# Kernel optimization log

Measured on AMD Instinct MI355X. Metric: run time of the kernel, lower is better.

Reference implementation:

```python
import jax, jax.numpy as jnp
import numpy as np

# Dims: C cells, L gene tokens, E embed, H mlp hidden, M factors, K topk
C, L, E, H, M, K = 16, 8192, 512, 256, 128, 30
TAU = 1.0        # gumbel-softmax temperature
SOFTNESS = 0.01  # soft-mask sharpness
TEMP = 1.0       # logits temperature
EPS = 1e-20


def setup_inputs() -> dict:
    key = jax.random.key(0)
    ks = jax.random.split(key, 7)
    x = jax.random.normal(ks[0], (C, L, E), dtype=jnp.float32)
    key_padding_mask = jax.random.randint(ks[1], (C, L), 0, 2) > 0  # True = valid
    uniform_noise = jax.random.uniform(ks[2], (C, L - 1, M), dtype=jnp.float32)
    W1 = jax.random.normal(ks[3], (E, H), dtype=jnp.float32) * (1.0 / np.sqrt(E))
    b1 = jnp.zeros((H,), dtype=jnp.float32)
    W2 = jax.random.normal(ks[4], (H, M), dtype=jnp.float32) * (1.0 / np.sqrt(H))
    b2 = jnp.zeros((M,), dtype=jnp.float32)
    return {"x": x, "key_padding_mask": key_padding_mask,
            "uniform_noise": uniform_noise,
            "W1": W1, "b1": b1, "W2": W2, "b2": b2}


def reference(x, key_padding_mask, uniform_noise, W1, b1, W2, b2):
    # default gene_subset: drop token 0, keep the rest  -> S = L-1
    xs = x[:, 1:, :]                          # (C, S, E)
    kpm = key_padding_mask[:, 1:]             # (C, S)

    # 2-layer MLP router (dropout p=0 -> identity)
    h = jax.nn.relu(jnp.einsum('cse,eh->csh', xs, W1) + b1)   # (C, S, H)
    logits = (jnp.einsum('csh,hm->csm', h, W2) + b2) / TEMP    # (C, S, M)

    # GumbelTopK, training path: gumbel-softmax then smooth top-k mask
    gumbel = -jnp.log(-jnp.log(uniform_noise + EPS) + EPS)
    perturbed = (logits + gumbel) / TAU
    probs = jax.nn.softmax(perturbed, axis=-1)                 # (C, S, M)
    topk_vals, _ = jax.lax.top_k(probs, K)                     # (C, S, K)
    threshold = topk_vals[..., -1:]                            # (C, S, 1)
    smooth_mask = jax.nn.sigmoid((probs - threshold) / SOFTNESS)
    out = probs * smooth_mask

    # faithful to the source: mask = ~key_padding_mask; probs *= mask
    out = out * (~kpm)[..., None].astype(out.dtype)
    return out, kpm
```

## Files before the change

### kernel.cpp

```cpp
#include <hip/hip_runtime.h>
#include <hip/hip_bf16.h>

#define CC 16
#define LL 8192
#define SS 8191
#define EE 512
#define HH 256
#define MM 128
#define TOPK 30

typedef __attribute__((ext_vector_type(8))) short short8;
typedef __attribute__((ext_vector_type(4))) float f32x4;
typedef __attribute__((ext_vector_type(4))) unsigned int u32x4;

static __device__ __forceinline__ unsigned short f2bf(float f) {
    unsigned u = __builtin_bit_cast(unsigned, f);
    u += 0x7FFFu + ((u >> 16) & 1u);
    return (unsigned short)(u >> 16);
}

static __device__ __forceinline__ unsigned pk2(float lo, float hi) {
    __hip_bfloat162 t = __float22bfloat162_rn(float2{lo, hi});
    unsigned u;
    __builtin_memcpy(&u, &t, 4);
    return u;
}

static __device__ __forceinline__ short8 cvt8(const float4 a, const float4 b) {
    u32x4 uv;
    uv[0] = pk2(a.x, a.y);
    uv[1] = pk2(a.z, a.w);
    uv[2] = pk2(b.x, b.y);
    uv[3] = pk2(b.z, b.w);
    return __builtin_bit_cast(short8, uv);
}

static __device__ __forceinline__ void gl2lds16(const float* g, unsigned char* l) {
    __builtin_amdgcn_global_load_lds(
        (const __attribute__((address_space(1))) void*)g,
        (__attribute__((address_space(3))) void*)l,
        16, 0, 0);
}

template<int CTRL>
static __device__ __forceinline__ float dppf(float v) {
    return __builtin_bit_cast(float,
        __builtin_amdgcn_update_dpp(0, __builtin_bit_cast(int, v), CTRL, 0xF, 0xF, false));
}
template<int CTRL>
static __device__ __forceinline__ int dppi(int v) {
    return __builtin_amdgcn_update_dpp(0, v, CTRL, 0xF, 0xF, false);
}
static __device__ __forceinline__ float sum16f(float v) {
    v += dppf<0x121>(v); v += dppf<0x122>(v); v += dppf<0x124>(v); v += dppf<0x128>(v);
    return v;
}
static __device__ __forceinline__ float max16f(float v) {
    v = fmaxf(v, dppf<0x121>(v)); v = fmaxf(v, dppf<0x122>(v));
    v = fmaxf(v, dppf<0x124>(v)); v = fmaxf(v, dppf<0x128>(v));
    return v;
}
static __device__ __forceinline__ unsigned sum16u(unsigned v) {
    v += (unsigned)dppi<0x121>((int)v); v += (unsigned)dppi<0x122>((int)v);
    v += (unsigned)dppi<0x124>((int)v); v += (unsigned)dppi<0x128>((int)v);
    return v;
}

__global__ void prep_weights(const float* __restrict__ W1, const float* __restrict__ W2,
                             unsigned short* __restrict__ W1T, unsigned short* __restrict__ W2T)
{
    const int b = blockIdx.x, tid = threadIdx.x;
    if (b < 64) {
        const int e0 = b * 8, h = tid;
        short8 sv;
#pragma unroll
        for (int j = 0; j < 8; ++j)
            sv[j] = (short)f2bf(W1[(size_t)(e0 + j) * HH + h]);
        *(short8*)(void*)(W1T + (size_t)h * EE + e0) = sv;
    } else {
        const int h0 = (b - 64) * 16;
        if (tid < MM) {
            const int m = tid;
            short8 s0v, s1v;
#pragma unroll
            for (int j = 0; j < 8; ++j) {
                s0v[j] = (short)f2bf(W2[(size_t)(h0 + j) * MM + m]);
                s1v[j] = (short)f2bf(W2[(size_t)(h0 + 8 + j) * MM + m]);
            }
            *(short8*)(void*)(W2T + (size_t)m * HH + h0) = s0v;
            *(short8*)(void*)(W2T + (size_t)m * HH + h0 + 8) = s1v;
        }
    }
}

__global__ __launch_bounds__(512, 4)
void gene_router_kernel(const float* __restrict__ x,
                        const int*   __restrict__ mask,
                        const float* __restrict__ noise,
                        const unsigned short* __restrict__ W1T,
                        const float* __restrict__ b1,
                        const unsigned short* __restrict__ W2T,
                        const float* __restrict__ b2,
                        float* __restrict__ out,
                        float* __restrict__ outk)
{
    __shared__ __align__(16) unsigned char lds[65536];

    const int tid = threadIdx.x;
    const int c   = blockIdx.y;
    const int s0  = blockIdx.x * 128;

    const int w    = tid >> 6;
    const int lane = tid & 63;
    const int lr   = lane & 15;
    const int kq   = lane >> 4;
    const int wr   = w >> 2;
    const int wc   = w & 3;
    const int tx   = tid & 15;
    const int ty   = tid >> 4;

    if (tid < 128) {
        const int s = s0 + tid;
        if (s < SS)
            outk[(size_t)c * SS + s] = (mask[(size_t)c * LL + s + 1] != 0) ? 1.0f : 0.0f;
    }

    const float* xb = x + ((size_t)c * LL + s0 + 1) * EE;

#define STAGE(ck, bufoff) do {                                              \
    _Pragma("unroll")                                                       \
    for (int it_ = 0; it_ < 4; ++it_) {                                     \
        const int row_ = it_ * 32 + ty;                                     \
        const int rs_  = min(s0 + row_, SS - 1) - s0;                       \
        const float* g_ = xb + (size_t)rs_ * EE + (ck) * 64                 \
                          + ((tx ^ (row_ & 7)) << 2);                       \
        gl2lds16(g_, lds + (bufoff) + (it_ * 512 + tid) * 16);              \
    } } while (0)

    const int cw = wc * 64;
    float b1v[4];
#pragma unroll
    for (int n = 0; n < 4; ++n) b1v[n] = b1[cw + n * 16 + lr];

    f32x4 acc[4][4];
#pragma unroll
    for (int r = 0; r < 4; ++r)
#pragma unroll
        for (int n = 0; n < 4; ++n) acc[r][n] = (f32x4)0.0f;

    STAGE(0, 0);
    __syncthreads();

    for (int ck = 0; ck < 8; ++ck) {
        const int cur = (ck & 1) << 15;
        if (ck < 7) STAGE(ck + 1, ((ck + 1) & 1) << 15);
#pragma unroll
        for (int ks = 0; ks < 2; ++ks) {
            short8 af[4];
#pragma unroll
            for (int r = 0; r < 4; ++r) {
                const int row = wr * 64 + r * 16 + lr;
                const int ug  = ks * 8 + kq * 2;
                const float4 a0 = *(const float4*)(const void*)
                    (lds + cur + row * 256 + (((ug + 0) ^ (row & 7)) << 4));
                const float4 a1 = *(const float4*)(const void*)
                    (lds + cur + row * 256 + (((ug + 1) ^ (row & 7)) << 4));
                af[r] = cvt8(a0, a1);
            }
            short8 bf_[4];
#pragma unroll
            for (int n = 0; n < 4; ++n)
                bf_[n] = *(const short8*)(const void*)
                    (W1T + (size_t)(cw + n * 16 + lr) * EE + ck * 64 + ks * 32 + kq * 8);
#pragma unroll
            for (int r = 0; r < 4; ++r)
#pragma unroll
                for (int n = 0; n < 4; ++n)
                    acc[r][n] = __builtin_amdgcn_mfma_f32_16x16x32_bf16(af[r], bf_[n], acc[r][n], 0, 0, 0);
        }
        __syncthreads();
    }

#pragma unroll
    for (int n = 0; n < 4; ++n) {
        const int colh = cw + n * 16 + lr;
#pragma unroll
        for (int r = 0; r < 4; ++r)
#pragma unroll
            for (int q = 0; q < 4; ++q) {
                const int row = wr * 64 + r * 16 + kq * 4 + q;
                *(unsigned short*)(lds + row * 512 + ((colh * 2) ^ ((row & 7) << 4))) =
                    f2bf(fmaxf(acc[r][n][q] + b1v[n], 0.0f));
            }
    }
    __syncthreads();

    float4 nz[4][2];
    int mk[4];
#pragma unroll
    for (int i = 0; i < 4; ++i) {
        const int s  = s0 + ty * 4 + i;
        const int sc = min(s, SS - 1);
        const float* np_ = noise + ((size_t)c * SS + sc) * MM + tx * 8;
        nz[i][0] = *(const float4*)np_;
        nz[i][1] = *(const float4*)(np_ + 4);
        mk[i] = mask[(size_t)c * LL + sc + 1];
    }
    const float4 b2a = *(const float4*)(b2 + tx * 8);
    const float4 b2b = *(const float4*)(b2 + tx * 8 + 4);

    f32x4 acc2[4][2];
#pragma unroll
    for (int r = 0; r < 4; ++r)
#pragma unroll
        for (int n = 0; n < 2; ++n) acc2[r][n] = (f32x4)0.0f;

    const int cw2 = wc * 32;
#pragma unroll 4
    for (int ks = 0; ks < 8; ++ks) {
        short8 ah[4];
#pragma unroll
        for (int r = 0; r < 4; ++r) {
            const int row = wr * 64 + r * 16 + lr;
            ah[r] = *(const short8*)(const void*)
                (lds + row * 512 + ((ks * 64 + kq * 16) ^ ((row & 7) << 4)));
        }
        short8 bw[2];
#pragma unroll
        for (int n = 0; n < 2; ++n)
            bw[n] = *(const short8*)(const void*)
                (W2T + (size_t)(cw2 + n * 16 + lr) * HH + ks * 32 + kq * 8);
#pragma unroll
        for (int r = 0; r < 4; ++r)
#pragma unroll
            for (int n = 0; n < 2; ++n)
                acc2[r][n] = __builtin_amdgcn_mfma_f32_16x16x32_bf16(ah[r], bw[n], acc2[r][n], 0, 0, 0);
    }
    __syncthreads();

#pragma unroll
    for (int r = 0; r < 4; ++r)
#pragma unroll
        for (int n = 0; n < 2; ++n)
#pragma unroll
            for (int q = 0; q < 4; ++q) {
                const int row = wr * 64 + r * 16 + kq * 4 + q;
                const int col = cw2 + n * 16 + lr;
                *(float*)(lds + row * 512
                          + ((((col >> 2) << 4) ^ ((row & 7) << 4)) | ((col & 3) << 2)))
                    = acc2[r][n][q];
            }
    __syncthreads();

    float b2v[8] = {b2a.x, b2a.y, b2a.z, b2a.w, b2b.x, b2b.y, b2b.z, b2b.w};

    float pr[4][8];
    float pmaxv[4];
#pragma unroll
    for (int i = 0; i < 4; ++i) {
        const int row = ty * 4 + i;
        const float4 l0 = *(const float4*)(const void*)
            (lds + row * 512 + ((tx * 32) ^ ((row & 7) << 4)));
        const float4 l1 = *(const float4*)(const void*)
            (lds + row * 512 + ((tx * 32 + 16) ^ ((row & 7) << 4)));
        const float lg[8] = {l0.x, l0.y, l0.z, l0.w, l1.x, l1.y, l1.z, l1.w};
        const float uu[8] = {nz[i][0].x, nz[i][0].y, nz[i][0].z, nz[i][0].w,
                             nz[i][1].x, nz[i][1].y, nz[i][1].z, nz[i][1].w};
        float pm[8];
#pragma unroll
        for (int q = 0; q < 8; ++q) {
            const float g = -__logf(-__logf(uu[q] + 1e-20f) + 1e-20f);
            pm[q] = lg[q] + b2v[q] + g;
        }
        float mx = pm[0];
#pragma unroll
        for (int q = 1; q < 8; ++q) mx = fmaxf(mx, pm[q]);
        mx = max16f(mx);
        float se = 0.0f;
#pragma unroll
        for (int q = 0; q < 8; ++q) { pr[i][q] = __expf(pm[q] - mx); se += pr[i][q]; }
        se = sum16f(se);
        const float inv = 1.0f / se;
#pragma unroll
        for (int q = 0; q < 8; ++q) pr[i][q] *= inv;
        pmaxv[i] = inv;
    }

    float lo[4], hi[4];
#pragma unroll
    for (int i = 0; i < 4; ++i) { lo[i] = 0.0f; hi[i] = fminf(pmaxv[i], 1.0f / 30.0f); }
    for (int it = 0; it < 16; ++it) {
        float mid[4];
#pragma unroll
        for (int i = 0; i < 4; ++i) mid[i] = 0.5f * (lo[i] + hi[i]);
        unsigned cnt = 0;
#pragma unroll
        for (int q = 0; q < 8; ++q) {
            cnt += (pr[0][q] > mid[0]) ? 1u : 0u;
            cnt += (pr[1][q] > mid[1]) ? (1u << 8) : 0u;
            cnt += (pr[2][q] > mid[2]) ? (1u << 16) : 0u;
            cnt += (pr[3][q] > mid[3]) ? (1u << 24) : 0u;
        }
        cnt = sum16u(cnt);
#pragma unroll
        for (int i = 0; i < 4; ++i) {
            const bool ge = ((cnt >> (8 * i)) & 255u) >= TOPK;
            lo[i] = ge ? mid[i] : lo[i];
            hi[i] = ge ? hi[i] : mid[i];
        }
    }

#pragma unroll
    for (int i = 0; i < 4; ++i) {
        const int s = s0 + ty * 4 + i;
        if (s < SS) {
            const float mz = (mk[i] != 0) ? 0.0f : 1.0f;
            float ov[8];
#pragma unroll
            for (int q = 0; q < 8; ++q) {
                const float sm = 1.0f / (1.0f + __expf((hi[i] - pr[i][q]) * 100.0f));
                ov[q] = pr[i][q] * sm * mz;
            }
            float* op = out + ((size_t)c * SS + s) * MM + tx * 8;
            float4 o0, o1;
            o0.x=ov[0]; o0.y=ov[1]; o0.z=ov[2]; o0.w=ov[3];
            o1.x=ov[4]; o1.y=ov[5]; o1.z=ov[6]; o1.w=ov[7];
            *(float4*)(op + 0) = o0;
            *(float4*)(op + 4) = o1;
        }
    }
#undef STAGE
}

extern "C" void kernel_launch(void* const* d_in, const int* in_sizes, int n_in,
                              void* d_out, int out_size, void* d_ws, size_t ws_size,
                              hipStream_t stream) {
    const float* x     = (const float*)d_in[0];
    const int*   mask  = (const int*)d_in[1];
    const float* noise = (const float*)d_in[2];
    const float* W1    = (const float*)d_in[3];
    const float* b1    = (const float*)d_in[4];
    const float* W2    = (const float*)d_in[5];
    const float* b2    = (const float*)d_in[6];
    float* out  = (float*)d_out;
    float* outk = out + (size_t)CC * SS * MM;

    unsigned short* W1T = (unsigned short*)d_ws;
    unsigned short* W2T = W1T + (size_t)HH * EE;

    prep_weights<<<dim3(80), dim3(256), 0, stream>>>(W1, W2, W1T, W2T);

    dim3 grid(64, CC);
    gene_router_kernel<<<grid, dim3(512), 0, stream>>>(x, mask, noise, W1T, b1, W2T, b2, out, outk);
}
```

Measured before the change: 181.0 us.

## Deepen x staging to 4-buffer ring with vmcnt waits and lighter barriers

Replaces the double-buffered 64-column x staging with a 4-slot ring of 32-column chunks, keeping three chunks in flight and waiting with explicit s_waitcnt vmcnt counts instead of full syncthreads. Later __syncthreads calls become raw s_barrier plus an lgkmcnt wait with sched_barrier fences. The aim is to hide global-to-LDS latency behind the MFMA work and cut barrier overhead. In exchange there are twice as many barriers in the K loop, a hand-tuned wait schedule that must match the issued loads exactly, and reduced scheduler freedom.

```diff
diff --git a/kernel.cpp b/kernel.cpp
--- a/kernel.cpp
+++ b/kernel.cpp
@@ -64,6 +64,18 @@
     v += (unsigned)dppi<0x121>((int)v); v += (unsigned)dppi<0x122>((int)v);
     v += (unsigned)dppi<0x124>((int)v); v += (unsigned)dppi<0x128>((int)v);
     return v;
+}
+
+static __device__ __forceinline__ void bar_only() {
+    __builtin_amdgcn_sched_barrier(0);
+    __builtin_amdgcn_s_barrier();
+    __builtin_amdgcn_sched_barrier(0);
+}
+static __device__ __forceinline__ void bar_lgkm() {
+    asm volatile("s_waitcnt lgkmcnt(0)" ::: "memory");
+    __builtin_amdgcn_sched_barrier(0);
+    __builtin_amdgcn_s_barrier();
+    __builtin_amdgcn_sched_barrier(0);
 }
 
 __global__ void prep_weights(const float* __restrict__ W1, const float* __restrict__ W2,
@@ -127,14 +139,16 @@
 
     const float* xb = x + ((size_t)c * LL + s0 + 1) * EE;
 
-#define STAGE(ck, bufoff) do {                                              \
+#define STAGE(ck) do {                                                      \
+    const int bo_ = ((ck) & 3) * 16384;                                     \
     _Pragma("unroll")                                                       \
-    for (int it_ = 0; it_ < 4; ++it_) {                                     \
-        const int row_ = it_ * 32 + ty;                                     \
+    for (int j_ = 0; j_ < 2; ++j_) {                                        \
+        const int unit_ = j_ * 512 + tid;                                   \
+        const int row_ = unit_ >> 3, uu_ = unit_ & 7;                       \
         const int rs_  = min(s0 + row_, SS - 1) - s0;                       \
-        const float* g_ = xb + (size_t)rs_ * EE + (ck) * 64                 \
-                          + ((tx ^ (row_ & 7)) << 2);                       \
-        gl2lds16(g_, lds + (bufoff) + (it_ * 512 + tid) * 16);              \
+        const float* g_ = xb + (size_t)rs_ * EE + (ck) * 32                 \
+                          + ((uu_ ^ (row_ & 7)) << 2);                      \
+        gl2lds16(g_, lds + bo_ + unit_ * 16);                               \
     } } while (0)
 
     const int cw = wc * 64;
@@ -148,38 +162,44 @@
 #pragma unroll
         for (int n = 0; n < 4; ++n) acc[r][n] = (f32x4)0.0f;
 
-    STAGE(0, 0);
-    __syncthreads();
-
-    for (int ck = 0; ck < 8; ++ck) {
-        const int cur = (ck & 1) << 15;
-        if (ck < 7) STAGE(ck + 1, ((ck + 1) & 1) << 15);
-#pragma unroll
-        for (int ks = 0; ks < 2; ++ks) {
-            short8 af[4];
-#pragma unroll
-            for (int r = 0; r < 4; ++r) {
-                const int row = wr * 64 + r * 16 + lr;
-                const int ug  = ks * 8 + kq * 2;
-                const float4 a0 = *(const float4*)(const void*)
-                    (lds + cur + row * 256 + (((ug + 0) ^ (row & 7)) << 4));
-                const float4 a1 = *(const float4*)(const void*)
-                    (lds + cur + row * 256 + (((ug + 1) ^ (row & 7)) << 4));
-                af[r] = cvt8(a0, a1);
-            }
-            short8 bf_[4];
-#pragma unroll
-            for (int n = 0; n < 4; ++n)
-                bf_[n] = *(const short8*)(const void*)
-                    (W1T + (size_t)(cw + n * 16 + lr) * EE + ck * 64 + ks * 32 + kq * 8);
-#pragma unroll
-            for (int r = 0; r < 4; ++r)
-#pragma unroll
-                for (int n = 0; n < 4; ++n)
-                    acc[r][n] = __builtin_amdgcn_mfma_f32_16x16x32_bf16(af[r], bf_[n], acc[r][n], 0, 0, 0);
-        }
-        __syncthreads();
-    }
+    STAGE(0); STAGE(1); STAGE(2);
+
+#define DO_CHUNK(C, W) do {                                                 \
+    asm volatile("s_waitcnt vmcnt(" #W ")" ::: "memory");                   \
+    __builtin_amdgcn_sched_barrier(0);                                      \
+    __builtin_amdgcn_s_barrier();                                           \
+    __builtin_amdgcn_sched_barrier(0);                                      \
+    if ((C) < 13) STAGE((C) + 3);                                           \
+    const unsigned char* cb_ = lds + ((C) & 3) * 16384;                     \
+    short8 af_[4];                                                          \
+    _Pragma("unroll")                                                       \
+    for (int r_ = 0; r_ < 4; ++r_) {                                        \
+        const int row_ = wr * 64 + r_ * 16 + lr;                            \
+        const float4 a0_ = *(const float4*)(const void*)                    \
+            (cb_ + row_ * 128 + (((kq * 2 + 0) ^ (row_ & 7)) << 4));        \
+        const float4 a1_ = *(const float4*)(const void*)                    \
+            (cb_ + row_ * 128 + (((kq * 2 + 1) ^ (row_ & 7)) << 4));        \
+        af_[r_] = cvt8(a0_, a1_);                                           \
+    }                                                                       \
+    short8 bw_[4];                                                          \
+    _Pragma("unroll")                                                       \
+    for (int n_ = 0; n_ < 4; ++n_)                                          \
+        bw_[n_] = *(const short8*)(const void*)                             \
+            (W1T + (size_t)(cw + n_ * 16 + lr) * EE + (C) * 32 + kq * 8);   \
+    _Pragma("unroll")                                                       \
+    for (int r_ = 0; r_ < 4; ++r_)                                          \
+        _Pragma("unroll")                                                   \
+        for (int n_ = 0; n_ < 4; ++n_)                                      \
+            acc[r_][n_] = __builtin_amdgcn_mfma_f32_16x16x32_bf16(          \
+                af_[r_], bw_[n_], acc[r_][n_], 0, 0, 0);                    \
+    } while (0)
+
+    DO_CHUNK( 0, 4); DO_CHUNK( 1, 4); DO_CHUNK( 2, 4); DO_CHUNK( 3, 4);
+    DO_CHUNK( 4, 4); DO_CHUNK( 5, 4); DO_CHUNK( 6, 4); DO_CHUNK( 7, 4);
+    DO_CHUNK( 8, 4); DO_CHUNK( 9, 4); DO_CHUNK(10, 4); DO_CHUNK(11, 4);
+    DO_CHUNK(12, 4); DO_CHUNK(13, 4); DO_CHUNK(14, 2); DO_CHUNK(15, 0);
+
+    bar_only();
 
 #pragma unroll
     for (int n = 0; n < 4; ++n) {
@@ -193,7 +213,7 @@
                     f2bf(fmaxf(acc[r][n][q] + b1v[n], 0.0f));
             }
     }
-    __syncthreads();
+    bar_lgkm();
 
     float4 nz[4][2];
     int mk[4];
@@ -236,7 +256,7 @@
             for (int n = 0; n < 2; ++n)
                 acc2[r][n] = __builtin_amdgcn_mfma_f32_16x16x32_bf16(ah[r], bw[n], acc2[r][n], 0, 0, 0);
     }
-    __syncthreads();
+    bar_lgkm();
 
 #pragma unroll
     for (int r = 0; r < 4; ++r)
@@ -250,7 +270,7 @@
                           + ((((col >> 2) << 4) ^ ((row & 7) << 4)) | ((col & 3) << 2)))
                     = acc2[r][n][q];
             }
-    __syncthreads();
+    bar_lgkm();
 
     float b2v[8] = {b2a.x, b2a.y, b2a.z, b2a.w, b2b.x, b2b.y, b2b.z, b2b.w};
 
@@ -329,6 +349,7 @@
             *(float4*)(op + 4) = o1;
         }
     }
+#undef DO_CHUNK
 #undef STAGE
 }
 
```

Result: slower. 186.2 us (+2.9%).

## Split fused router into GEMM kernel and separate softmax/top-k epilogue kernel

Applied to the files above, without the earlier changes.

Splits the single fused kernel into two. The first does the MLP GEMMs and writes raw logits to the output buffer. The second reads logits and noise back and does the gumbel-softmax, the top-k threshold search and the masking. The aim is to shed register and LDS pressure from the epilogue in the GEMM kernel and run the epilogue at higher occupancy. The cost is an extra global round trip of the logits, about 67 MB. The bisection is also cut from 16 to 10 iterations, which coarsens the threshold and may change numerics.

```diff
diff --git a/kernel.cpp b/kernel.cpp
--- a/kernel.cpp
+++ b/kernel.cpp
@@ -8,6 +8,7 @@
 #define HH 256
 #define MM 128
 #define TOPK 30
+#define TOT (CC * SS)
 
 typedef __attribute__((ext_vector_type(8))) short short8;
 typedef __attribute__((ext_vector_type(4))) float f32x4;
@@ -94,15 +95,11 @@
 }
 
 __global__ __launch_bounds__(512, 4)
-void gene_router_kernel(const float* __restrict__ x,
-                        const int*   __restrict__ mask,
-                        const float* __restrict__ noise,
-                        const unsigned short* __restrict__ W1T,
-                        const float* __restrict__ b1,
-                        const unsigned short* __restrict__ W2T,
-                        const float* __restrict__ b2,
-                        float* __restrict__ out,
-                        float* __restrict__ outk)
+void gene_gemm_kernel(const float* __restrict__ x,
+                      const unsigned short* __restrict__ W1T,
+                      const float* __restrict__ b1,
+                      const unsigned short* __restrict__ W2T,
+                      float* __restrict__ logits)
 {
     __shared__ __align__(16) unsigned char lds[65536];
 
@@ -118,12 +115,6 @@
     const int wc   = w & 3;
     const int tx   = tid & 15;
     const int ty   = tid >> 4;
-
-    if (tid < 128) {
-        const int s = s0 + tid;
-        if (s < SS)
-            outk[(size_t)c * SS + s] = (mask[(size_t)c * LL + s + 1] != 0) ? 1.0f : 0.0f;
-    }
 
     const float* xb = x + ((size_t)c * LL + s0 + 1) * EE;
 
@@ -195,20 +186,6 @@
     }
     __syncthreads();
 
-    float4 nz[4][2];
-    int mk[4];
-#pragma unroll
-    for (int i = 0; i < 4; ++i) {
-        const int s  = s0 + ty * 4 + i;
-        const int sc = min(s, SS - 1);
-        const float* np_ = noise + ((size_t)c * SS + sc) * MM + tx * 8;
-        nz[i][0] = *(const float4*)np_;
-        nz[i][1] = *(const float4*)(np_ + 4);
-        mk[i] = mask[(size_t)c * LL + sc + 1];
-    }
-    const float4 b2a = *(const float4*)(b2 + tx * 8);
-    const float4 b2b = *(const float4*)(b2 + tx * 8 + 4);
-
     f32x4 acc2[4][2];
 #pragma unroll
     for (int r = 0; r < 4; ++r)
@@ -236,7 +213,6 @@
             for (int n = 0; n < 2; ++n)
                 acc2[r][n] = __builtin_amdgcn_mfma_f32_16x16x32_bf16(ah[r], bw[n], acc2[r][n], 0, 0, 0);
     }
-    __syncthreads();
 
 #pragma unroll
     for (int r = 0; r < 4; ++r)
@@ -244,28 +220,62 @@
         for (int n = 0; n < 2; ++n)
 #pragma unroll
             for (int q = 0; q < 4; ++q) {
-                const int row = wr * 64 + r * 16 + kq * 4 + q;
-                const int col = cw2 + n * 16 + lr;
-                *(float*)(lds + row * 512
-                          + ((((col >> 2) << 4) ^ ((row & 7) << 4)) | ((col & 3) << 2)))
-                    = acc2[r][n][q];
-            }
-    __syncthreads();
-
-    float b2v[8] = {b2a.x, b2a.y, b2a.z, b2a.w, b2b.x, b2b.y, b2b.z, b2b.w};
+                const int s = s0 + wr * 64 + r * 16 + kq * 4 + q;
+                if (s < SS)
+                    logits[((size_t)c * SS + s) * MM + cw2 + n * 16 + lr] = acc2[r][n][q];
+            }
+#undef STAGE
+}
+
+__global__ __launch_bounds__(256, 8)
+void gene_epi_kernel(const float* __restrict__ noise,
+                     const int*   __restrict__ mask,
+                     const float* __restrict__ b2,
+                     float* __restrict__ out,
+                     float* __restrict__ outk)
+{
+    const int tid = threadIdx.x;
+    const int tx  = tid & 15;
+    const int ty  = tid >> 4;
+    const long base = (long)blockIdx.x * 64;
+
+    if (tid < 64) {
+        const long gr = base + tid;
+        if (gr < TOT) {
+            const int cc2 = (int)(gr / SS);
+            outk[gr] = (mask[gr + cc2 + 1] != 0) ? 1.0f : 0.0f;
+        }
+    }
+
+    float b2v[8];
+    {
+        const float4 bb0 = *(const float4*)(b2 + tx * 8 + 0);
+        const float4 bb1 = *(const float4*)(b2 + tx * 8 + 4);
+        b2v[0]=bb0.x; b2v[1]=bb0.y; b2v[2]=bb0.z; b2v[3]=bb0.w;
+        b2v[4]=bb1.x; b2v[5]=bb1.y; b2v[6]=bb1.z; b2v[7]=bb1.w;
+    }
 
     float pr[4][8];
     float pmaxv[4];
+    float mz[4];
+    long  grv[4];
+
 #pragma unroll
     for (int i = 0; i < 4; ++i) {
-        const int row = ty * 4 + i;
-        const float4 l0 = *(const float4*)(const void*)
-            (lds + row * 512 + ((tx * 32) ^ ((row & 7) << 4)));
-        const float4 l1 = *(const float4*)(const void*)
-            (lds + row * 512 + ((tx * 32 + 16) ^ ((row & 7) << 4)));
-        const float lg[8] = {l0.x, l0.y, l0.z, l0.w, l1.x, l1.y, l1.z, l1.w};
-        const float uu[8] = {nz[i][0].x, nz[i][0].y, nz[i][0].z, nz[i][0].w,
-                             nz[i][1].x, nz[i][1].y, nz[i][1].z, nz[i][1].w};
+        const long gr  = base + ty * 4 + i;
+        grv[i] = gr;
+        const long grc = gr < TOT ? gr : (TOT - 1);
+        const int  cc2 = (int)(grc / SS);
+        mz[i] = (mask[grc + cc2 + 1] != 0) ? 0.0f : 1.0f;
+
+        const float* lp = out   + grc * MM + tx * 8;
+        const float* np = noise + grc * MM + tx * 8;
+        const float4 l0 = *(const float4*)lp;
+        const float4 l1 = *(const float4*)(lp + 4);
+        const float4 u0 = *(const float4*)np;
+        const float4 u1 = *(const float4*)(np + 4);
+        const float lg[8] = {l0.x,l0.y,l0.z,l0.w,l1.x,l1.y,l1.z,l1.w};
+        const float uu[8] = {u0.x,u0.y,u0.z,u0.w,u1.x,u1.y,u1.z,u1.w};
         float pm[8];
 #pragma unroll
         for (int q = 0; q < 8; ++q) {
@@ -289,7 +299,7 @@
     float lo[4], hi[4];
 #pragma unroll
     for (int i = 0; i < 4; ++i) { lo[i] = 0.0f; hi[i] = fminf(pmaxv[i], 1.0f / 30.0f); }
-    for (int it = 0; it < 16; ++it) {
+    for (int it = 0; it < 10; ++it) {
         float mid[4];
 #pragma unroll
         for (int i = 0; i < 4; ++i) mid[i] = 0.5f * (lo[i] + hi[i]);
@@ -312,16 +322,14 @@
 
 #pragma unroll
     for (int i = 0; i < 4; ++i) {
-        const int s = s0 + ty * 4 + i;
-        if (s < SS) {
-            const float mz = (mk[i] != 0) ? 0.0f : 1.0f;
+        if (grv[i] < TOT) {
             float ov[8];
 #pragma unroll
             for (int q = 0; q < 8; ++q) {
                 const float sm = 1.0f / (1.0f + __expf((hi[i] - pr[i][q]) * 100.0f));
-                ov[q] = pr[i][q] * sm * mz;
-            }
-            float* op = out + ((size_t)c * SS + s) * MM + tx * 8;
+                ov[q] = pr[i][q] * sm * mz[i];
+            }
+            float* op = out + grv[i] * MM + tx * 8;
             float4 o0, o1;
             o0.x=ov[0]; o0.y=ov[1]; o0.z=ov[2]; o0.w=ov[3];
             o1.x=ov[4]; o1.y=ov[5]; o1.z=ov[6]; o1.w=ov[7];
@@ -329,7 +337,6 @@
             *(float4*)(op + 4) = o1;
         }
     }
-#undef STAGE
 }
 
 extern "C" void kernel_launch(void* const* d_in, const int* in_sizes, int n_in,
@@ -350,6 +357,8 @@
 
     prep_weights<<<dim3(80), dim3(256), 0, stream>>>(W1, W2, W1T, W2T);
 
-    dim3 grid(64, CC);
-    gene_router_kernel<<<grid, dim3(512), 0, stream>>>(x, mask, noise, W1T, b1, W2T, b2, out, outk);
-}
+    gene_gemm_kernel<<<dim3(64, CC), dim3(512), 0, stream>>>(x, W1T, b1, W2T, out);
+
+    const int nblk = (TOT + 63) / 64;
+    gene_epi_kernel<<<dim3(nblk), dim3(256), 0, stream>>>(noise, mask, b2, out, outk);
+}
```

New measurement: 177.1 us. 1.02x faster.
